# Kernel tuning notes

Hardware: AMD Instinct MI355X
Metric: run time of the kernel (lower is better)

## Reference

```python
import jax, jax.numpy as jnp
import numpy as np

BETA = 0.25
NUM_EMBEDS = 1024
EMBED_DIM = 256


def setup_inputs() -> dict:
    key = jax.random.key(0)
    k1, k2 = jax.random.split(key)
    z_e = jax.random.normal(k1, (32, EMBED_DIM, 1024), dtype=jnp.float32)
    lim = 1.0 / NUM_EMBEDS
    embed_weight = jax.random.uniform(k2, (NUM_EMBEDS, EMBED_DIM), dtype=jnp.float32,
                                      minval=-lim, maxval=lim)
    return {"z_e": z_e, "embed_weight": embed_weight}


def reference(z_e, embed_weight):
    # z_e: (b, d, t) -> (b, t, d)
    ze = jnp.transpose(z_e, (0, 2, 1))
    b, t, d = ze.shape
    flat = ze.reshape(-1, d)  # (N, d)
    K = embed_weight.shape[0]
    # squared euclidean distances (N, K) via sum-of-squares + matmul
    distances = (jnp.sum(flat ** 2, axis=1, keepdims=True)
                 + jnp.sum(embed_weight ** 2, axis=1)
                 - 2.0 * flat @ embed_weight.T)
    idx = jnp.argmin(distances, axis=1)  # (N,)
    # one-hot @ W is just a gather
    z_q = embed_weight[idx].reshape(b, t, d)
    # commitment / codebook losses (mse over all elements)
    e_latent_loss = jnp.mean((jax.lax.stop_gradient(z_q) - ze) ** 2)
    q_latent_loss = jnp.mean((z_q - jax.lax.stop_gradient(ze)) ** 2)
    reg_loss = q_latent_loss + BETA * e_latent_loss
    # straight-through estimator
    z_q_st = ze + jax.lax.stop_gradient(z_q - ze)
    z_q_out = jnp.transpose(z_q_st, (0, 2, 1))  # (b, d, t)
    # perplexity from codebook usage
    N = flat.shape[0]
    avg_probs = jnp.zeros((K,), dtype=jnp.float32).at[idx].add(1.0) / N
    perplexity = jnp.exp(-jnp.sum(avg_probs * jnp.log(avg_probs + 1e-10)))
    return (z_q_out, reg_loss, perplexity)
```

## Files before the change

kernel.cpp:

```cpp
#include <hip/hip_runtime.h>
#include <math.h>

#define BB 32
#define DD 256
#define TT 1024
#define KK 1024
#define NN (BB*TT)

#define BROWS 64
#define CCH   256
#define DSL   64
#define NSTEP 16


__global__ void prep_kernel(const float* __restrict__ W, float* __restrict__ wsq,
                            int* __restrict__ counts, float* __restrict__ sse) {
    const int k = blockIdx.x;
    const int lane = threadIdx.x;
    const float4 v = ((const float4*)(W + (size_t)k * DD))[lane];
    double s = (double)v.x * v.x + (double)v.y * v.y + (double)v.z * v.z + (double)v.w * v.w;
    #pragma unroll
    for (int m = 32; m > 0; m >>= 1) s += __shfl_down(s, m);
    if (lane == 0) wsq[k] = (float)s;
    if (blockIdx.x < 16) counts[blockIdx.x * 64 + lane] = 0;
    if (blockIdx.x == 0 && lane == 0) *sse = 0.0f;
}

__device__ __forceinline__ int swz_w(int r, int q) { return r * 16 + (q ^ ((r >> 3) & 7)); }
__device__ __forceinline__ int swz_z(int r, int q) { return r * 16 + (q ^ (r & 7) ^ ((r >> 3) & 7)); }

__device__ __forceinline__ void gl_lds16(const float* g, void* l) {
    __builtin_amdgcn_global_load_lds((const __attribute__((address_space(1))) void*)g,
                                     (__attribute__((address_space(3))) void*)l, 16, 0, 0);
}

__global__ __launch_bounds__(256, 2) void vq_fused_kernel(
    const float* __restrict__ z, const float* __restrict__ W,
    const float* __restrict__ wsq, float* __restrict__ out,
    int* __restrict__ counts, float* __restrict__ sse)
{
    __shared__ float4 zs[BROWS * 16];
    __shared__ float4 ws[CCH * 16];
    const int tid = threadIdx.x;
    const int tx = tid & 31, ty = tid >> 5;
    const int w = tid >> 6, lane = tid & 63;
    const int row0 = blockIdx.x * BROWS;
    const int b = row0 >> 10, t0 = row0 & 1023;
    const size_t bbase = (size_t)b * DD * TT;
    const float* zbase = z + bbase + t0;

    float rsq[8];
    {
        const int ro = lane & 15;
        const int g  = lane >> 4;
        const float* zp = zbase + (size_t)g * 64 * TT + (16 * w + ro);
        double s = 0.0;
        #pragma unroll 4
        for (int d = 0; d < 64; ++d) { float v = zp[(size_t)d * TT]; s += (double)v * v; }
        s += __shfl_xor(s, 16);
        s += __shfl_xor(s, 32);
        float f = (float)s;
        #pragma unroll
        for (int i = 0; i < 8; ++i) rsq[i] = __shfl(f, (ty & 1) * 8 + i);
    }

    float minv[8]; int mini[8];
    #pragma unroll
    for (int i = 0; i < 8; ++i) { minv[i] = 3.4e38f; mini[i] = 0; }

    const int zr = tid & 63;
    const int zq0 = w * 4;
    float4 zreg[4];
    {
        #pragma unroll
        for (int j = 0; j < 4; ++j) {
            const float* zp = zbase + (size_t)((zq0 + j) * 4) * TT + zr;
            zreg[j].x = zp[0]; zreg[j].y = zp[(size_t)TT];
            zreg[j].z = zp[(size_t)2 * TT]; zreg[j].w = zp[(size_t)3 * TT];
        }
    }

    const int wr0 = w * 64 + (lane >> 4);
    const int wslot = lane & 15;
    char* const wlbase = (char*)ws + (size_t)w * 16384;

    float acc[8][8];
    float wq[8];

    for (int s = 0; s < NSTEP; ++s) {
        const int sl = s & 3, ch = s >> 2;
        __syncthreads();
        #pragma unroll
        for (int j = 0; j < 4; ++j) zs[swz_z(zr, zq0 + j)] = zreg[j];
        {
            const float* wch = W + (size_t)(ch * CCH) * DD + sl * DSL;
            #pragma unroll
            for (int k = 0; k < 16; ++k) {
                int r = wr0 + k * 4;
                const float* g = wch + (size_t)r * DD + 4 * (wslot ^ ((r >> 3) & 7));
                gl_lds16(g, wlbase + k * 1024);
            }
        }
        __syncthreads();

        if (sl == 0) {
            #pragma unroll
            for (int i = 0; i < 8; ++i)
                #pragma unroll
                for (int j = 0; j < 8; ++j) acc[i][j] = 0.0f;
            #pragma unroll
            for (int j = 0; j < 8; ++j) wq[j] = wsq[ch * CCH + tx * 8 + j];
        }
        if (s < NSTEP - 1) {
            const int sln = (s + 1) & 3;
            #pragma unroll
            for (int j = 0; j < 4; ++j) {
                const float* zp = zbase + (size_t)(sln * DSL + (zq0 + j) * 4) * TT + zr;
                zreg[j].x = zp[0]; zreg[j].y = zp[(size_t)TT];
                zreg[j].z = zp[(size_t)2 * TT]; zreg[j].w = zp[(size_t)3 * TT];
            }
        }
        for (int q = 0; q < 16; ++q) {
            float4 zf[8], wf[8];
            #pragma unroll
            for (int i = 0; i < 8; ++i) zf[i] = zs[swz_z(ty * 8 + i, q)];
            #pragma unroll
            for (int j = 0; j < 8; ++j) wf[j] = ws[swz_w(tx * 8 + j, q)];
            #pragma unroll
            for (int i = 0; i < 8; ++i)
                #pragma unroll
                for (int j = 0; j < 8; ++j) {
                    acc[i][j] = fmaf(zf[i].x, wf[j].x, acc[i][j]);
                    acc[i][j] = fmaf(zf[i].y, wf[j].y, acc[i][j]);
                    acc[i][j] = fmaf(zf[i].z, wf[j].z, acc[i][j]);
                    acc[i][j] = fmaf(zf[i].w, wf[j].w, acc[i][j]);
                }
        }
        if (sl == 3) {
            #pragma unroll
            for (int j = 0; j < 8; ++j) {
                int c = ch * CCH + tx * 8 + j;
                #pragma unroll
                for (int i = 0; i < 8; ++i) {
                    float s1 = rsq[i] + wq[j];
                    float v = fmaf(-2.0f, acc[i][j], s1);
                    if (v < minv[i]) { minv[i] = v; mini[i] = c; }
                }
            }
        }
    }

    __syncthreads();
    int* idxs = (int*)zs;
    float* ssescr = (float*)zs + 64;
    #pragma unroll
    for (int i = 0; i < 8; ++i) {
        float v = minv[i]; int ix = mini[i];
        #pragma unroll
        for (int m = 1; m < 32; m <<= 1) {
            float ov = __shfl_xor(v, m);
            int   oi = __shfl_xor(ix, m);
            if (ov < v || (ov == v && oi < ix)) { v = ov; ix = oi; }
        }
        if (tx == 0) {
            idxs[ty * 8 + i] = ix;
            atomicAdd(&counts[ix], 1);
        }
    }
    __syncthreads();

    const int tg = tid & 15;
    const int dg = tid >> 4;
    const int t4 = tg * 4;
    int ixs[4];
    #pragma unroll
    for (int m = 0; m < 4; ++m) ixs[m] = idxs[t4 + m];
    float ssel = 0.0f;
    #pragma unroll
    for (int k4 = 0; k4 < 4; ++k4) {
        const int d0 = dg * 16 + k4 * 4;
        float wr[4][4];
        #pragma unroll
        for (int m = 0; m < 4; ++m) {
            float4 wv = *(const float4*)(W + (size_t)ixs[m] * DD + d0);
            wr[m][0] = wv.x; wr[m][1] = wv.y; wr[m][2] = wv.z; wr[m][3] = wv.w;
        }
        #pragma unroll
        for (int dd = 0; dd < 4; ++dd) {
            const int d = d0 + dd;
            const size_t base = bbase + (size_t)d * TT + t0 + t4;
            float4 zv = *(const float4*)(z + base);
            float e0 = wr[0][dd] - zv.x, e1 = wr[1][dd] - zv.y;
            float e2 = wr[2][dd] - zv.z, e3 = wr[3][dd] - zv.w;
            float4 o;
            o.x = zv.x + e0; o.y = zv.y + e1; o.z = zv.z + e2; o.w = zv.w + e3;
            *(float4*)(out + base) = o;
            ssel += (e0 * e0 + e1 * e1) + (e2 * e2 + e3 * e3);
        }
    }
    #pragma unroll
    for (int m = 32; m > 0; m >>= 1) ssel += __shfl_down(ssel, m);
    if (lane == 0) ssescr[w] = ssel;
    __syncthreads();
    if (tid == 0) atomicAdd(sse, (ssescr[0] + ssescr[1]) + (ssescr[2] + ssescr[3]));
}

__global__ void finalize_kernel(const int* __restrict__ counts, const float* __restrict__ sse,
                                float* __restrict__ out) {
    float s = 0.0f;
    for (int k = threadIdx.x; k < KK; k += 256) {
        float p = (float)counts[k] / (float)NN;
        s += p * logf(p + 1e-10f);
    }
    #pragma unroll
    for (int m = 32; m > 0; m >>= 1) s += __shfl_down(s, m);
    __shared__ float wsum[4];
    if ((threadIdx.x & 63) == 0) wsum[threadIdx.x >> 6] = s;
    __syncthreads();
    if (threadIdx.x == 0) {
        float ent = (wsum[0] + wsum[1]) + (wsum[2] + wsum[3]);
        out[(size_t)BB * DD * TT]     = 1.25f * (*sse) / (float)(BB * DD * TT);
        out[(size_t)BB * DD * TT + 1] = expf(-ent);
    }
}

extern "C" void kernel_launch(void* const* d_in, const int* in_sizes, int n_in,
                              void* d_out, int out_size, void* d_ws, size_t ws_size,
                              hipStream_t stream) {
    const float* z = (const float*)d_in[0];
    const float* W = (const float*)d_in[1];
    float* out = (float*)d_out;

    float* wsq    = (float*)d_ws;
    int*   counts = (int*)(wsq + 1024);
    float* sse    = (float*)(counts + 1024);

    prep_kernel<<<1024, 64, 0, stream>>>(W, wsq, counts, sse);
    vq_fused_kernel<<<NN / BROWS, 256, 0, stream>>>(z, W, wsq, out, counts, sse);
    finalize_kernel<<<1, 256, 0, stream>>>(counts, sse, out);
}
```

Baseline: 272.2 us.

## Split codebook across two blocks per row tile with atomic argmin and separate output kernel

The fused VQ kernel is split into an argmin kernel and an output kernel. Each 64-row tile is now handled by two blocks that each cover half of the codebook, doubling the grid to 1024 blocks. Per-row minima are combined with a packed 64-bit atomicMin (distance bits in the high word, index in the low word). The argmin loop now double-buffers both z and W tiles in LDS with direct global-to-LDS loads, uses an 8x32 thread layout with an outer-product inner loop, raises launch bounds to 3 blocks per SM and sets wave priority around the FMA loop. The gain is more parallelism and better load overlap, at the cost of an extra kernel launch, recomputing row norms in both blocks, and reading z again in a separate pass.

```diff
diff --git a/kernel.cpp b/kernel.cpp
--- a/kernel.cpp
+++ b/kernel.cpp
@@ -7,14 +7,14 @@
 #define KK 1024
 #define NN (BB*TT)
 
-#define BROWS 64
-#define CCH   256
-#define DSL   64
-#define NSTEP 16
-
+#define NSTEP 32
+
+
+typedef unsigned long long u64;
 
 __global__ void prep_kernel(const float* __restrict__ W, float* __restrict__ wsq,
-                            int* __restrict__ counts, float* __restrict__ sse) {
+                            int* __restrict__ counts, float* __restrict__ sse,
+                            u64* __restrict__ rowbest) {
     const int k = blockIdx.x;
     const int lane = threadIdx.x;
     const float4 v = ((const float4*)(W + (size_t)k * DD))[lane];
@@ -24,122 +24,132 @@
     if (lane == 0) wsq[k] = (float)s;
     if (blockIdx.x < 16) counts[blockIdx.x * 64 + lane] = 0;
     if (blockIdx.x == 0 && lane == 0) *sse = 0.0f;
-}
-
-__device__ __forceinline__ int swz_w(int r, int q) { return r * 16 + (q ^ ((r >> 3) & 7)); }
-__device__ __forceinline__ int swz_z(int r, int q) { return r * 16 + (q ^ (r & 7) ^ ((r >> 3) & 7)); }
+    const int gid = blockIdx.x * 64 + lane;
+    if (gid < NN) rowbest[gid] = ~0ull;
+}
 
 __device__ __forceinline__ void gl_lds16(const float* g, void* l) {
     __builtin_amdgcn_global_load_lds((const __attribute__((address_space(1))) void*)g,
                                      (__attribute__((address_space(3))) void*)l, 16, 0, 0);
 }
 
-__global__ __launch_bounds__(256, 2) void vq_fused_kernel(
+__global__ __launch_bounds__(256, 3) void vq_argmin_kernel(
     const float* __restrict__ z, const float* __restrict__ W,
-    const float* __restrict__ wsq, float* __restrict__ out,
-    int* __restrict__ counts, float* __restrict__ sse)
+    const float* __restrict__ wsq, u64* __restrict__ rowbest)
 {
-    __shared__ float4 zs[BROWS * 16];
-    __shared__ float4 ws[CCH * 16];
+    __shared__ float  zst[2][32 * 64];
+    __shared__ float4 wst[2][256 * 4];
     const int tid = threadIdx.x;
-    const int tx = tid & 31, ty = tid >> 5;
+    const int tx = tid & 7, ty = tid >> 3;
     const int w = tid >> 6, lane = tid & 63;
-    const int row0 = blockIdx.x * BROWS;
+    const int rb = blockIdx.x >> 1, cb = blockIdx.x & 1;
+    const int row0 = rb * 64, C0 = cb * 512;
     const int b = row0 >> 10, t0 = row0 & 1023;
-    const size_t bbase = (size_t)b * DD * TT;
-    const float* zbase = z + bbase + t0;
+    const float* zbase = z + (size_t)b * DD * TT + t0;
 
     float rsq[8];
     {
-        const int ro = lane & 15;
-        const int g  = lane >> 4;
-        const float* zp = zbase + (size_t)g * 64 * TT + (16 * w + ro);
+        double* pscr = (double*)&wst[0][0];
+        float*  fscr = (float*)&zst[1][0];
+        const int rr = tid & 63, g = tid >> 6;
+        const float* zp = zbase + (size_t)g * 64 * TT + rr;
         double s = 0.0;
         #pragma unroll 4
         for (int d = 0; d < 64; ++d) { float v = zp[(size_t)d * TT]; s += (double)v * v; }
-        s += __shfl_xor(s, 16);
-        s += __shfl_xor(s, 32);
-        float f = (float)s;
-        #pragma unroll
-        for (int i = 0; i < 8; ++i) rsq[i] = __shfl(f, (ty & 1) * 8 + i);
+        pscr[g * 64 + rr] = s;
+        __syncthreads();
+        if (tid < 64)
+            fscr[tid] = (float)((pscr[tid] + pscr[64 + tid]) + (pscr[128 + tid] + pscr[192 + tid]));
+        __syncthreads();
+        #pragma unroll
+        for (int i = 0; i < 8; ++i) rsq[i] = fscr[tx * 8 + i];
+        __syncthreads();
+    }
+
+    {
+        const float* wc = W + (size_t)C0 * DD;
+        #pragma unroll
+        for (int k = 0; k < 4; ++k) {
+            const int idx = k * 256 + tid, c = idx >> 2, s = idx & 3;
+            gl_lds16(wc + (size_t)c * DD + 4 * (s ^ ((c >> 3) & 3)),
+                     (char*)&wst[0][0] + (size_t)idx * 16);
+        }
+        #pragma unroll
+        for (int k = 0; k < 2; ++k) {
+            const int idx = k * 256 + tid, d = idx >> 4, r4 = (idx & 15) * 4;
+            gl_lds16(zbase + (size_t)d * TT + r4, (char*)&zst[0][0] + (size_t)idx * 16);
+        }
     }
 
     float minv[8]; int mini[8];
     #pragma unroll
     for (int i = 0; i < 8; ++i) { minv[i] = 3.4e38f; mini[i] = 0; }
-
-    const int zr = tid & 63;
-    const int zq0 = w * 4;
-    float4 zreg[4];
-    {
-        #pragma unroll
-        for (int j = 0; j < 4; ++j) {
-            const float* zp = zbase + (size_t)((zq0 + j) * 4) * TT + zr;
-            zreg[j].x = zp[0]; zreg[j].y = zp[(size_t)TT];
-            zreg[j].z = zp[(size_t)2 * TT]; zreg[j].w = zp[(size_t)3 * TT];
-        }
-    }
-
-    const int wr0 = w * 64 + (lane >> 4);
-    const int wslot = lane & 15;
-    char* const wlbase = (char*)ws + (size_t)w * 16384;
-
     float acc[8][8];
     float wq[8];
 
-    for (int s = 0; s < NSTEP; ++s) {
-        const int sl = s & 3, ch = s >> 2;
-        __syncthreads();
-        #pragma unroll
-        for (int j = 0; j < 4; ++j) zs[swz_z(zr, zq0 + j)] = zreg[j];
-        {
-            const float* wch = W + (size_t)(ch * CCH) * DD + sl * DSL;
-            #pragma unroll
-            for (int k = 0; k < 16; ++k) {
-                int r = wr0 + k * 4;
-                const float* g = wch + (size_t)r * DD + 4 * (wslot ^ ((r >> 3) & 7));
-                gl_lds16(g, wlbase + k * 1024);
-            }
-        }
-        __syncthreads();
-
+    for (int t = 0; t < NSTEP; ++t) {
+        const int sl = t & 15, ch = t >> 4, h = t & 1;
+        asm volatile("s_waitcnt vmcnt(0)" ::: "memory");
+        __syncthreads();
+        if (t + 1 < NSTEP) {
+            const int tn = t + 1;
+            const float* wc = W + (size_t)(C0 + (tn >> 4) * 256) * DD + (tn & 15) * 16;
+            #pragma unroll
+            for (int k = 0; k < 4; ++k) {
+                const int idx = k * 256 + tid, c = idx >> 2, s = idx & 3;
+                gl_lds16(wc + (size_t)c * DD + 4 * (s ^ ((c >> 3) & 3)),
+                         (char*)&wst[tn & 1][0] + (size_t)idx * 16);
+            }
+        }
+        if ((t & 1) == 0 && t + 2 < NSTEP) {
+            const int dn = ((t + 2) & 15) * 16;
+            char* dst = (char*)&zst[((t + 2) >> 1) & 1][0];
+            #pragma unroll
+            for (int k = 0; k < 2; ++k) {
+                const int idx = k * 256 + tid, d = idx >> 4, r4 = (idx & 15) * 4;
+                gl_lds16(zbase + (size_t)(dn + d) * TT + r4, dst + (size_t)idx * 16);
+            }
+        }
         if (sl == 0) {
             #pragma unroll
             for (int i = 0; i < 8; ++i)
                 #pragma unroll
                 for (int j = 0; j < 8; ++j) acc[i][j] = 0.0f;
             #pragma unroll
-            for (int j = 0; j < 8; ++j) wq[j] = wsq[ch * CCH + tx * 8 + j];
-        }
-        if (s < NSTEP - 1) {
-            const int sln = (s + 1) & 3;
-            #pragma unroll
-            for (int j = 0; j < 4; ++j) {
-                const float* zp = zbase + (size_t)(sln * DSL + (zq0 + j) * 4) * TT + zr;
-                zreg[j].x = zp[0]; zreg[j].y = zp[(size_t)TT];
-                zreg[j].z = zp[(size_t)2 * TT]; zreg[j].w = zp[(size_t)3 * TT];
-            }
-        }
-        for (int q = 0; q < 16; ++q) {
-            float4 zf[8], wf[8];
-            #pragma unroll
-            for (int i = 0; i < 8; ++i) zf[i] = zs[swz_z(ty * 8 + i, q)];
-            #pragma unroll
-            for (int j = 0; j < 8; ++j) wf[j] = ws[swz_w(tx * 8 + j, q)];
-            #pragma unroll
-            for (int i = 0; i < 8; ++i)
+            for (int j = 0; j < 8; ++j) wq[j] = wsq[C0 + ch * 256 + ty * 8 + j];
+        }
+        const float*  zb = &zst[(t >> 1) & 1][h * 16 * 64];
+        const float4* wb = &wst[h][ty * 32];
+        __builtin_amdgcn_s_setprio(1);
+        for (int q = 0; q < 4; ++q) {
+            float4 wf[8];
+            const float4* wp = wb + (q ^ (ty & 3));
+            #pragma unroll
+            for (int j = 0; j < 8; ++j) wf[j] = wp[j * 4];
+            #pragma unroll
+            for (int dp = 0; dp < 4; ++dp) {
+                const float4* zp = (const float4*)(zb + (q * 4 + dp) * 64 + tx * 8);
+                const float4 za = zp[0], zc = zp[1];
                 #pragma unroll
                 for (int j = 0; j < 8; ++j) {
-                    acc[i][j] = fmaf(zf[i].x, wf[j].x, acc[i][j]);
-                    acc[i][j] = fmaf(zf[i].y, wf[j].y, acc[i][j]);
-                    acc[i][j] = fmaf(zf[i].z, wf[j].z, acc[i][j]);
-                    acc[i][j] = fmaf(zf[i].w, wf[j].w, acc[i][j]);
+                    const float wv = dp == 0 ? wf[j].x : dp == 1 ? wf[j].y
+                                   : dp == 2 ? wf[j].z : wf[j].w;
+                    acc[0][j] = fmaf(za.x, wv, acc[0][j]);
+                    acc[1][j] = fmaf(za.y, wv, acc[1][j]);
+                    acc[2][j] = fmaf(za.z, wv, acc[2][j]);
+                    acc[3][j] = fmaf(za.w, wv, acc[3][j]);
+                    acc[4][j] = fmaf(zc.x, wv, acc[4][j]);
+                    acc[5][j] = fmaf(zc.y, wv, acc[5][j]);
+                    acc[6][j] = fmaf(zc.z, wv, acc[6][j]);
+                    acc[7][j] = fmaf(zc.w, wv, acc[7][j]);
                 }
-        }
-        if (sl == 3) {
+            }
+        }
+        __builtin_amdgcn_s_setprio(0);
+        if (sl == 15) {
             #pragma unroll
             for (int j = 0; j < 8; ++j) {
-                int c = ch * CCH + tx * 8 + j;
+                const int c = C0 + ch * 256 + ty * 8 + j;
                 #pragma unroll
                 for (int i = 0; i < 8; ++i) {
                     float s1 = rsq[i] + wq[j];
@@ -151,24 +161,48 @@
     }
 
     __syncthreads();
-    int* idxs = (int*)zs;
-    float* ssescr = (float*)zs + 64;
+    float* cvs = (float*)&zst[0][0];
+    int*   cis = (int*)&zst[0][0] + 256;
     #pragma unroll
     for (int i = 0; i < 8; ++i) {
         float v = minv[i]; int ix = mini[i];
         #pragma unroll
-        for (int m = 1; m < 32; m <<= 1) {
+        for (int m = 8; m < 64; m <<= 1) {
             float ov = __shfl_xor(v, m);
             int   oi = __shfl_xor(ix, m);
             if (ov < v || (ov == v && oi < ix)) { v = ov; ix = oi; }
         }
-        if (tx == 0) {
-            idxs[ty * 8 + i] = ix;
-            atomicAdd(&counts[ix], 1);
-        }
-    }
-    __syncthreads();
-
+        if (lane < 8) { cvs[w * 64 + lane * 8 + i] = v; cis[w * 64 + lane * 8 + i] = ix; }
+    }
+    __syncthreads();
+    if (tid < 64) {
+        float bv = cvs[tid]; int bi = cis[tid];
+        #pragma unroll
+        for (int ww = 1; ww < 4; ++ww) {
+            float v = cvs[ww * 64 + tid]; int ii = cis[ww * 64 + tid];
+            if (v < bv || (v == bv && ii < bi)) { bv = v; bi = ii; }
+        }
+        const u64 key = ((u64)__float_as_uint(bv) << 32) | (unsigned)bi;
+        atomicMin(&rowbest[row0 + tid], key);
+    }
+}
+
+__global__ void vq_out_kernel(const float* __restrict__ z, const float* __restrict__ W,
+                              const u64* __restrict__ rowbest, float* __restrict__ out,
+                              int* __restrict__ counts, float* __restrict__ sse) {
+    __shared__ int idxs[64];
+    __shared__ float ssescr[4];
+    const int tid = threadIdx.x;
+    const int w = tid >> 6;
+    const int row0 = blockIdx.x * 64;
+    const int b = row0 >> 10, t0 = row0 & 1023;
+    const size_t bbase = (size_t)b * DD * TT;
+    if (tid < 64) {
+        const int ix = (int)(rowbest[row0 + tid] & 0xffffffffull);
+        idxs[tid] = ix;
+        atomicAdd(&counts[ix], 1);
+    }
+    __syncthreads();
     const int tg = tid & 15;
     const int dg = tid >> 4;
     const int t4 = tg * 4;
@@ -200,7 +234,7 @@
     }
     #pragma unroll
     for (int m = 32; m > 0; m >>= 1) ssel += __shfl_down(ssel, m);
-    if (lane == 0) ssescr[w] = ssel;
+    if ((tid & 63) == 0) ssescr[w] = ssel;
     __syncthreads();
     if (tid == 0) atomicAdd(sse, (ssescr[0] + ssescr[1]) + (ssescr[2] + ssescr[3]));
 }
@@ -234,8 +268,10 @@
     float* wsq    = (float*)d_ws;
     int*   counts = (int*)(wsq + 1024);
     float* sse    = (float*)(counts + 1024);
-
-    prep_kernel<<<1024, 64, 0, stream>>>(W, wsq, counts, sse);
-    vq_fused_kernel<<<NN / BROWS, 256, 0, stream>>>(z, W, wsq, out, counts, sse);
+    u64*   rowbest = (u64*)((float*)d_ws + 2052);
+
+    prep_kernel<<<1024, 64, 0, stream>>>(W, wsq, counts, sse, rowbest);
+    vq_argmin_kernel<<<1024, 256, 0, stream>>>(z, W, wsq, rowbest);
+    vq_out_kernel<<<512, 256, 0, stream>>>(z, W, rowbest, out, counts, sse);
     finalize_kernel<<<1, 256, 0, stream>>>(counts, sse, out);
 }
```

New measurement: 975.6 us. 258% more time.
